# Performance work log

Hardware: AMD Instinct MI355X
Metric: run time of the kernel (lower is better)

## Reference

```python
import jax, jax.numpy as jnp
import numpy as np

N_NODES = 100000
N_EDGES = 3200000
N_GRAPHS = 64


def _gcn_conv(x, W, b, row, col, norm, n):
    # GCNConv: linear transform, then normalized scatter-add aggregation, then bias
    h = x @ W                                  # [N, H]
    msg = h[row] * norm[:, None]               # gather + scale, [E+N, H]
    out = jax.ops.segment_sum(msg, col, num_segments=n)
    return out + b


def setup_inputs() -> dict:
    key = jax.random.key(0)
    ks = jax.random.split(key, 8)
    x = jax.random.normal(ks[0], (N_NODES, 128), dtype=jnp.float32)
    edge_index = jax.random.randint(ks[1], (2, N_EDGES), 0, N_NODES, dtype=jnp.int64)
    batch = jnp.sort(jax.random.randint(ks[2], (N_NODES,), 0, N_GRAPHS, dtype=jnp.int64))
    W1 = jax.random.normal(ks[3], (128, 256), dtype=jnp.float32) * (1.0 / np.sqrt(128))
    b1 = jnp.zeros((256,), dtype=jnp.float32)
    W2 = jax.random.normal(ks[4], (256, 256), dtype=jnp.float32) * (1.0 / np.sqrt(256))
    b2 = jnp.zeros((256,), dtype=jnp.float32)
    Wl = jax.random.normal(ks[5], (256, 2), dtype=jnp.float32) * (1.0 / np.sqrt(256))
    bl = jnp.zeros((2,), dtype=jnp.float32)
    return {"x": x, "edge_index": edge_index, "batch": batch,
            "W1": W1, "b1": b1, "W2": W2, "b2": b2, "Wl": Wl, "bl": bl}


def reference(x, edge_index, batch, W1, b1, W2, b2, Wl, bl):
    n = x.shape[0]
    # add self-loops (PyG GCNConv default)
    loop = jnp.arange(n, dtype=edge_index.dtype)
    row = jnp.concatenate([edge_index[0], loop])   # source
    col = jnp.concatenate([edge_index[1], loop])   # target
    # symmetric normalization: deg computed on targets (with self-loops)
    deg = jax.ops.segment_sum(jnp.ones_like(col, dtype=x.dtype), col, num_segments=n)
    dinv = jnp.where(deg > 0, jax.lax.rsqrt(deg), 0.0)
    norm = dinv[row] * dinv[col]

    h = jax.nn.relu(_gcn_conv(x, W1, b1, row, col, norm, n))
    # dropout p=0.1 is identity at inference (training=False)
    h = jax.nn.relu(_gcn_conv(h, W2, b2, row, col, norm, n))

    # global mean pool over graphs
    sums = jax.ops.segment_sum(h, batch, num_segments=N_GRAPHS)
    cnts = jax.ops.segment_sum(jnp.ones((n,), dtype=h.dtype), batch, num_segments=N_GRAPHS)
    pooled = sums / jnp.maximum(cnts, 1.0)[:, None]

    return pooled @ Wl + bl
```

## Files before the change

### kernel.cpp

```cpp
#include <hip/hip_runtime.h>
#include <hip/hip_bf16.h>
#include <cstddef>

#define NODES  100000
#define EDGES  3200000
#define ETOT   3300000
#define NGRAPH 64
#define HDIM   256
#define BSHIFT 9
#define NBUCK  196
#define BCAP   19456

typedef __hip_bfloat16 bf16;
typedef short bf16x8 __attribute__((ext_vector_type(8)));
typedef float f32x4 __attribute__((ext_vector_type(4)));
typedef float f32x2 __attribute__((ext_vector_type(2)));
typedef unsigned u32x2 __attribute__((ext_vector_type(2)));
typedef unsigned u32x4 __attribute__((ext_vector_type(4)));

__device__ __forceinline__ float blo(unsigned u) { return __uint_as_float(u << 16); }
__device__ __forceinline__ float bhi(unsigned u) { return __uint_as_float(u & 0xffff0000u); }

__global__ void xcast_kernel(const float* __restrict__ x, bf16* __restrict__ xb) {
    int i = blockIdx.x * 256 + threadIdx.x;
    if ((size_t)i * 4 >= (size_t)NODES * 128) return;
    float4 v = *(const float4*)(x + (size_t)i * 4);
    union { __hip_bfloat162 h[2]; uint2 u; } pk;
    pk.h[0] = __float22bfloat162_rn(make_float2(v.x, v.y));
    pk.h[1] = __float22bfloat162_rn(make_float2(v.z, v.w));
    *(uint2*)(xb + (size_t)i * 4) = pk.u;
}

__global__ void wcast_kernel(const float* __restrict__ W1, const float* __restrict__ W2,
                             bf16* __restrict__ W1t, bf16* __restrict__ W2t) {
    int i = blockIdx.x * 256 + threadIdx.x;
    if (i < 128 * 256) {
        int n = i / 128, k = i - n * 128;
        W1t[i] = __float2bfloat16(W1[(size_t)k * 256 + n]);
    } else if (i < 128 * 256 + 256 * 256) {
        int q = i - 128 * 256;
        int n = q / 256, k = q - n * 256;
        W2t[q] = __float2bfloat16(W2[(size_t)k * 256 + n]);
    }
}

__global__ __launch_bounds__(1024) void fillp1_kernel(const int* __restrict__ row,
                                                      const int* __restrict__ col,
                                                      int* __restrict__ gcnt,
                                                      uint2* __restrict__ recs) {
    __shared__ int hist[NBUCK];
    __shared__ int base[NBUCK];
    int t = threadIdx.x;
    if (t < NBUCK) hist[t] = 0;
    __syncthreads();
    int e0 = blockIdx.x * 16384;
    int r[16], c[16], rk[16];
    #pragma unroll
    for (int i = 0; i < 16; i++) {
        int e = e0 + i * 1024 + t;
        r[i] = -1;
        if (e < ETOT) {
            if (e < EDGES) { r[i] = row[e]; c[i] = col[e]; }
            else           { r[i] = e - EDGES; c[i] = r[i]; }
            rk[i] = atomicAdd(&hist[c[i] >> BSHIFT], 1);
        }
    }
    __syncthreads();
    if (t < NBUCK && hist[t] > 0) base[t] = atomicAdd(&gcnt[t], hist[t]);
    __syncthreads();
    #pragma unroll
    for (int i = 0; i < 16; i++) {
        if (r[i] >= 0) {
            int b = c[i] >> BSHIFT;
            recs[(size_t)b * BCAP + base[b] + rk[i]] = make_uint2((unsigned)r[i], (unsigned)c[i]);
        }
    }
}

__global__ void bscan_kernel(const int* __restrict__ gcnt, int* __restrict__ bbase) {
    __shared__ int part[256];
    int t = threadIdx.x;
    int v0 = (t < NBUCK) ? gcnt[t] : 0;
    part[t] = v0;
    __syncthreads();
    for (int off = 1; off < 256; off <<= 1) {
        int v = (t >= off) ? part[t - off] : 0;
        __syncthreads();
        part[t] += v;
        __syncthreads();
    }
    if (t < NBUCK) bbase[t] = part[t] - v0;
}

__global__ __launch_bounds__(256) void build_kernel(const uint2* __restrict__ recs,
                                                    const int* __restrict__ gcnt,
                                                    const int* __restrict__ bbase,
                                                    int* __restrict__ rowptr,
                                                    float* __restrict__ dinv,
                                                    int* __restrict__ csr) {
    __shared__ int hist[512];
    __shared__ int cur[512];
    __shared__ int part[256];
    const int b = blockIdx.x, t = threadIdx.x;
    const int n0 = b << BSHIFT;
    const int cnt = gcnt[b];
    const int base = bbase[b];
    hist[t] = 0; hist[t + 256] = 0;
    __syncthreads();
    const uint2* rb = recs + (size_t)b * BCAP;
    for (int i = t; i < cnt; i += 256) atomicAdd(&hist[(int)rb[i].y - n0], 1);
    __syncthreads();
    int h0 = hist[2 * t], h1 = hist[2 * t + 1];
    part[t] = h0 + h1;
    __syncthreads();
    for (int off = 1; off < 256; off <<= 1) {
        int v = (t >= off) ? part[t - off] : 0;
        __syncthreads();
        part[t] += v;
        __syncthreads();
    }
    int ex = (t == 0) ? 0 : part[t - 1];
    cur[2 * t]     = ex;
    cur[2 * t + 1] = ex + h0;
    int v0 = n0 + 2 * t, v1 = v0 + 1;
    if (v0 < NODES) { rowptr[v0] = base + ex;      dinv[v0] = rsqrtf((float)h0); }
    if (v1 < NODES) { rowptr[v1] = base + ex + h0; dinv[v1] = rsqrtf((float)h1); }
    if (b == 0 && t == 0) rowptr[NODES] = ETOT;
    __syncthreads();
    for (int i = t; i < cnt; i += 256) {
        uint2 r = rb[i];
        int pos = atomicAdd(&cur[(int)r.y - n0], 1);
        csr[base + pos] = (int)r.x;
    }
}

__global__ void agg1_kernel(const bf16* __restrict__ xb, const int* __restrict__ rowptr,
                            const int* __restrict__ csr, const float* __restrict__ dinv,
                            bf16* __restrict__ out) {
    int w    = (blockIdx.x * blockDim.x + threadIdx.x) >> 6;
    int lane = threadIdx.x & 63;
    int half = lane >> 5, li = lane & 31;
    int node = w * 2 + half;
    if (node >= NODES) return;
    int beg = rowptr[node], end = rowptr[node + 1];
    float a0 = 0.f, a1 = 0.f, a2 = 0.f, a3 = 0.f;
    int j = beg;
    for (; j + 1 < end; j += 2) {
        int s0 = csr[j], s1 = csr[j + 1];
        float w0 = dinv[s0], w1 = dinv[s1];
        uint2 q0 = *(const uint2*)(xb + (size_t)s0 * 128 + li * 4);
        uint2 q1 = *(const uint2*)(xb + (size_t)s1 * 128 + li * 4);
        a0 += w0 * blo(q0.x) + w1 * blo(q1.x);
        a1 += w0 * bhi(q0.x) + w1 * bhi(q1.x);
        a2 += w0 * blo(q0.y) + w1 * blo(q1.y);
        a3 += w0 * bhi(q0.y) + w1 * bhi(q1.y);
    }
    if (j < end) {
        int s0 = csr[j];
        float w0 = dinv[s0];
        uint2 q0 = *(const uint2*)(xb + (size_t)s0 * 128 + li * 4);
        a0 += w0 * blo(q0.x);
        a1 += w0 * bhi(q0.x);
        a2 += w0 * blo(q0.y);
        a3 += w0 * bhi(q0.y);
    }
    float d = dinv[node];
    union { __hip_bfloat162 h[2]; uint2 u; } pk;
    pk.h[0] = __float22bfloat162_rn(make_float2(a0 * d, a1 * d));
    pk.h[1] = __float22bfloat162_rn(make_float2(a2 * d, a3 * d));
    *(uint2*)(out + (size_t)node * 128 + li * 4) = pk.u;
}

__global__ void agg2_kernel(const unsigned char* __restrict__ h8, const int* __restrict__ rowptr,
                            const int* __restrict__ csr, const float* __restrict__ dinv,
                            bf16* __restrict__ out) {
    int w    = (blockIdx.x * blockDim.x + threadIdx.x) >> 6;
    int lane = threadIdx.x & 63;
    int half = lane >> 5, li = lane & 31;
    int node = w * 2 + half;
    if (node >= NODES) return;
    int beg = rowptr[node], end = rowptr[node + 1];
    float a[8] = {};
    int j = beg;
#define ACC8(q, wv) do {                                                   \
        f32x2 d0 = __builtin_amdgcn_cvt_pk_f32_fp8((int)(q).x, false);     \
        f32x2 d1 = __builtin_amdgcn_cvt_pk_f32_fp8((int)(q).x, true);      \
        f32x2 d2 = __builtin_amdgcn_cvt_pk_f32_fp8((int)(q).y, false);     \
        f32x2 d3 = __builtin_amdgcn_cvt_pk_f32_fp8((int)(q).y, true);      \
        a[0] += (wv) * d0.x; a[1] += (wv) * d0.y;                          \
        a[2] += (wv) * d1.x; a[3] += (wv) * d1.y;                          \
        a[4] += (wv) * d2.x; a[5] += (wv) * d2.y;                          \
        a[6] += (wv) * d3.x; a[7] += (wv) * d3.y;                          \
    } while (0)
    for (; j + 3 < end; j += 4) {
        int s0 = csr[j], s1 = csr[j + 1], s2 = csr[j + 2], s3 = csr[j + 3];
        float w0 = dinv[s0], w1 = dinv[s1], w2 = dinv[s2], w3 = dinv[s3];
        u32x2 q0 = *(const u32x2*)(h8 + (size_t)s0 * 256 + li * 8);
        u32x2 q1 = *(const u32x2*)(h8 + (size_t)s1 * 256 + li * 8);
        u32x2 q2 = *(const u32x2*)(h8 + (size_t)s2 * 256 + li * 8);
        u32x2 q3 = *(const u32x2*)(h8 + (size_t)s3 * 256 + li * 8);
        ACC8(q0, w0); ACC8(q1, w1); ACC8(q2, w2); ACC8(q3, w3);
    }
    for (; j < end; j++) {
        int s0 = csr[j];
        float w0 = dinv[s0];
        u32x2 q0 = *(const u32x2*)(h8 + (size_t)s0 * 256 + li * 8);
        ACC8(q0, w0);
    }
#undef ACC8
    float d = dinv[node];
    union { __hip_bfloat162 h[4]; u32x4 u; } pk;
    pk.h[0] = __float22bfloat162_rn(make_float2(a[0] * d, a[1] * d));
    pk.h[1] = __float22bfloat162_rn(make_float2(a[2] * d, a[3] * d));
    pk.h[2] = __float22bfloat162_rn(make_float2(a[4] * d, a[5] * d));
    pk.h[3] = __float22bfloat162_rn(make_float2(a[6] * d, a[7] * d));
    *(u32x4*)(out + (size_t)node * 256 + li * 8) = pk.u;
}

template <int K, bool OUT_FP8>
__global__ __launch_bounds__(256) void mgemm_kernel(const bf16* __restrict__ A,
                                                    const bf16* __restrict__ Bt,
                                                    const float* __restrict__ bias,
                                                    bf16* __restrict__ Cb,
                                                    unsigned char* __restrict__ C8) {
    __shared__ short As[128][40];
    __shared__ short Bs[128][40];
    const int t    = threadIdx.x;
    const int bm   = (int)(blockIdx.x >> 1) * 128;
    const int bn   = (int)(blockIdx.x & 1) * 128;
    const int lane = t & 63;
    const int wave = t >> 6;
    const int wm   = (wave >> 1) * 64, wn = (wave & 1) * 64;
    const int m16  = lane & 15, kq = lane >> 4;
    f32x4 acc[4][4] = {};

    for (int k0 = 0; k0 < K; k0 += 32) {
        #pragma unroll
        for (int h = 0; h < 2; h++) {
            int q = t * 2 + h;
            int rr = q >> 2, seg = q & 3;
            uint4 va = {0u, 0u, 0u, 0u};
            int grow = bm + rr;
            if (grow < NODES) va = *(const uint4*)(A + (size_t)grow * K + k0 + seg * 8);
            *(uint4*)&As[rr][seg * 8] = va;
            uint4 vb = *(const uint4*)(Bt + (size_t)(bn + rr) * K + k0 + seg * 8);
            *(uint4*)&Bs[rr][seg * 8] = vb;
        }
        __syncthreads();
        bf16x8 af[4], bf_[4];
        #pragma unroll
        for (int i = 0; i < 4; i++) {
            af[i]  = *(const bf16x8*)&As[wm + i * 16 + m16][kq * 8];
            bf_[i] = *(const bf16x8*)&Bs[wn + i * 16 + m16][kq * 8];
        }
        #pragma unroll
        for (int mt = 0; mt < 4; mt++)
            #pragma unroll
            for (int nt = 0; nt < 4; nt++)
                acc[mt][nt] = __builtin_amdgcn_mfma_f32_16x16x32_bf16(af[mt], bf_[nt],
                                                                     acc[mt][nt], 0, 0, 0);
        __syncthreads();
    }

    #pragma unroll
    for (int mt = 0; mt < 4; mt++) {
        #pragma unroll
        for (int r = 0; r < 4; r++) {
            int row = bm + wm + mt * 16 + kq * 4 + r;
            if (row >= NODES) continue;
            #pragma unroll
            for (int nt = 0; nt < 4; nt++) {
                int colb = bn + wn + nt * 16 + m16;
                float v = fmaxf(acc[mt][nt][r] + bias[colb], 0.f);
                if (OUT_FP8) {
                    int pkd = __builtin_amdgcn_cvt_pk_fp8_f32(v, v, 0, false);
                    C8[(size_t)row * 256 + colb] = (unsigned char)(pkd & 0xff);
                } else {
                    Cb[(size_t)row * 256 + colb] = __float2bfloat16(v);
                }
            }
        }
    }
}

__global__ void pool_kernel(const bf16* __restrict__ h2, const int* __restrict__ batch,
                            float* __restrict__ sums) {
    int lane = threadIdx.x & 63;
    int sub  = threadIdx.x >> 6;
    int col  = blockIdx.y * 64 + lane;
    int r0   = blockIdx.x * 1024 + sub * 256;
    if (r0 >= NODES) return;
    int r1 = r0 + 256; if (r1 > NODES) r1 = NODES;
    float acc = 0.f;
    int g = batch[r0];
    for (int r = r0; r < r1; r++) {
        int gg = batch[r];
        if (gg != g) { atomicAdd(&sums[g * 256 + col], acc); acc = 0.f; g = gg; }
        acc += __bfloat162float(h2[(size_t)r * 256 + col]);
    }
    atomicAdd(&sums[g * 256 + col], acc);
}

__global__ void final_kernel(const float* __restrict__ sums, const int* __restrict__ batch,
                             const float* __restrict__ Wl, const float* __restrict__ bl,
                             float* __restrict__ out) {
    int g = blockIdx.x;
    int l = threadIdx.x;
    int lo = 0, hi = NODES;
    while (lo < hi) { int m = (lo + hi) >> 1; if (batch[m] < g) lo = m + 1; else hi = m; }
    int lb = lo;
    lo = lb; hi = NODES;
    while (lo < hi) { int m = (lo + hi) >> 1; if (batch[m] <= g) lo = m + 1; else hi = m; }
    int cnt = lo - lb;
    float inv = 1.f / fmaxf((float)cnt, 1.f);
    float a0 = 0.f, a1 = 0.f;
    for (int k = l; k < 256; k += 64) {
        float p = sums[g * 256 + k] * inv;
        a0 += p * Wl[k * 2 + 0];
        a1 += p * Wl[k * 2 + 1];
    }
    for (int off = 32; off > 0; off >>= 1) {
        a0 += __shfl_down(a0, off, 64);
        a1 += __shfl_down(a1, off, 64);
    }
    if (l == 0) {
        out[g * 2 + 0] = a0 + bl[0];
        out[g * 2 + 1] = a1 + bl[1];
    }
}

extern "C" void kernel_launch(void* const* d_in, const int* in_sizes, int n_in,
                              void* d_out, int out_size, void* d_ws, size_t ws_size,
                              hipStream_t stream) {
    const float* x    = (const float*)d_in[0];
    const int*   ei   = (const int*)d_in[1];
    const int*   bat  = (const int*)d_in[2];
    const float* W1   = (const float*)d_in[3];
    const float* b1   = (const float*)d_in[4];
    const float* W2   = (const float*)d_in[5];
    const float* b2   = (const float*)d_in[6];
    const float* Wl   = (const float*)d_in[7];
    const float* bl   = (const float*)d_in[8];
    float*       out  = (float*)d_out;
    const int* erow = ei;
    const int* ecol = ei + EDGES;

    char* p = (char*)d_ws;
    auto take = [&](size_t bytes) {
        char* r = p;
        p += (bytes + 255) & ~(size_t)255;
        return r;
    };
    float* dinv   = (float*)take((size_t)NODES * 4);
    int*   rowptr = (int*)  take((size_t)(NODES + 1) * 4);
    int*   gcnt   = (int*)  take((size_t)NBUCK * 4);
    int*   bbase  = (int*)  take((size_t)NBUCK * 4);
    int*   csr    = (int*)  take((size_t)ETOT * 4);
    float* sums   = (float*)take((size_t)NGRAPH * HDIM * 4);
    bf16*  W1t    = (bf16*) take((size_t)128 * 256 * 2);
    bf16*  W2t    = (bf16*) take((size_t)256 * 256 * 2);
    char*  reg1   = (char*) take((size_t)NODES * HDIM * 2);
    char*  reg2   = (char*) take((size_t)NODES * HDIM * 2);
    char*  reg3   = (char*) take((size_t)NODES * HDIM * 2);
    bf16*          xb      = (bf16*)reg1;
    unsigned char* h1f8    = (unsigned char*)reg1;
    bf16*          aggbuf1 = (bf16*)reg2;
    bf16*          aggbuf2 = (bf16*)reg2;
    uint2*         recs    = (uint2*)reg3;
    bf16*          h2b     = (bf16*)reg3;

    hipMemsetAsync(sums, 0, (size_t)NGRAPH * HDIM * 4, stream);
    hipMemsetAsync(gcnt, 0, (size_t)NBUCK * 4, stream);
    xcast_kernel<<<(NODES * 128 / 4 + 255) / 256, 256, 0, stream>>>(x, xb);
    wcast_kernel<<<(128 * 256 + 256 * 256 + 255) / 256, 256, 0, stream>>>(W1, W2, W1t, W2t);

    fillp1_kernel<<<(ETOT + 16383) / 16384, 1024, 0, stream>>>(erow, ecol, gcnt, recs);
    bscan_kernel <<<1, 256, 0, stream>>>(gcnt, bbase);
    build_kernel <<<NBUCK, 256, 0, stream>>>(recs, gcnt, bbase, rowptr, dinv, csr);

    const int AGG_BLOCKS = (NODES / 2 * 64) / 256;
    agg1_kernel<<<AGG_BLOCKS, 256, 0, stream>>>(xb, rowptr, csr, dinv, aggbuf1);

    const int MB = (NODES + 127) / 128;
    mgemm_kernel<128, true ><<<MB * 2, 256, 0, stream>>>(aggbuf1, W1t, b1, nullptr, h1f8);

    agg2_kernel<<<AGG_BLOCKS, 256, 0, stream>>>(h1f8, rowptr, csr, dinv, aggbuf2);

    mgemm_kernel<256, false><<<MB * 2, 256, 0, stream>>>(aggbuf2, W2t, b2, h2b, nullptr);

    pool_kernel<<<dim3((NODES + 1023) / 1024, 4), 256, 0, stream>>>(h2b, bat, sums);

    final_kernel<<<NGRAPH, 64, 0, stream>>>(sums, bat, Wl, bl, out);
}
```

Before: 626.0 us.

## Store input features and layer-2 output in fp8, split fill histogram four ways

Casts the input features to fp8 instead of bf16, so the first aggregation gathers half as many bytes per edge, and unrolls its edge loop by four. The second GEMM now writes fp8 instead of bf16, and pooling reads four fp8 values per lane. The bucket fill kernel spreads its shared-memory histogram atomics over four copies to reduce contention. These cuts in gather and write traffic cost extra quantization error on the input features and the final hidden state.

Result: faster. 560.8 us (-10.4%).

```diff
diff --git a/kernel.cpp b/kernel.cpp
--- a/kernel.cpp
+++ b/kernel.cpp
@@ -18,17 +18,13 @@
 typedef unsigned u32x2 __attribute__((ext_vector_type(2)));
 typedef unsigned u32x4 __attribute__((ext_vector_type(4)));
 
-__device__ __forceinline__ float blo(unsigned u) { return __uint_as_float(u << 16); }
-__device__ __forceinline__ float bhi(unsigned u) { return __uint_as_float(u & 0xffff0000u); }
-
-__global__ void xcast_kernel(const float* __restrict__ x, bf16* __restrict__ xb) {
+__global__ void xcast_kernel(const float* __restrict__ x, unsigned char* __restrict__ x8) {
     int i = blockIdx.x * 256 + threadIdx.x;
     if ((size_t)i * 4 >= (size_t)NODES * 128) return;
     float4 v = *(const float4*)(x + (size_t)i * 4);
-    union { __hip_bfloat162 h[2]; uint2 u; } pk;
-    pk.h[0] = __float22bfloat162_rn(make_float2(v.x, v.y));
-    pk.h[1] = __float22bfloat162_rn(make_float2(v.z, v.w));
-    *(uint2*)(xb + (size_t)i * 4) = pk.u;
+    int w = __builtin_amdgcn_cvt_pk_fp8_f32(v.x, v.y, 0, false);
+    w     = __builtin_amdgcn_cvt_pk_fp8_f32(v.z, v.w, w, true);
+    *(unsigned*)(x8 + (size_t)i * 4) = (unsigned)w;
 }
 
 __global__ void wcast_kernel(const float* __restrict__ W1, const float* __restrict__ W2,
@@ -48,10 +44,12 @@
                                                       const int* __restrict__ col,
                                                       int* __restrict__ gcnt,
                                                       uint2* __restrict__ recs) {
-    __shared__ int hist[NBUCK];
+    __shared__ int hist[4][NBUCK];
+    __shared__ int coff[4][NBUCK];
     __shared__ int base[NBUCK];
-    int t = threadIdx.x;
-    if (t < NBUCK) hist[t] = 0;
+    int t  = threadIdx.x;
+    int cp = t & 3;
+    for (int i = t; i < 4 * NBUCK; i += 1024) ((int*)hist)[i] = 0;
     __syncthreads();
     int e0 = blockIdx.x * 16384;
     int r[16], c[16], rk[16];
@@ -62,17 +60,23 @@
         if (e < ETOT) {
             if (e < EDGES) { r[i] = row[e]; c[i] = col[e]; }
             else           { r[i] = e - EDGES; c[i] = r[i]; }
-            rk[i] = atomicAdd(&hist[c[i] >> BSHIFT], 1);
-        }
-    }
-    __syncthreads();
-    if (t < NBUCK && hist[t] > 0) base[t] = atomicAdd(&gcnt[t], hist[t]);
+            rk[i] = atomicAdd(&hist[cp][c[i] >> BSHIFT], 1);
+        }
+    }
+    __syncthreads();
+    if (t < NBUCK) {
+        int h0 = hist[0][t], h1 = hist[1][t], h2 = hist[2][t], h3 = hist[3][t];
+        coff[0][t] = 0; coff[1][t] = h0; coff[2][t] = h0 + h1; coff[3][t] = h0 + h1 + h2;
+        int tot = h0 + h1 + h2 + h3;
+        base[t] = (tot > 0) ? atomicAdd(&gcnt[t], tot) : 0;
+    }
     __syncthreads();
     #pragma unroll
     for (int i = 0; i < 16; i++) {
         if (r[i] >= 0) {
             int b = c[i] >> BSHIFT;
-            recs[(size_t)b * BCAP + base[b] + rk[i]] = make_uint2((unsigned)r[i], (unsigned)c[i]);
+            recs[(size_t)b * BCAP + base[b] + coff[cp][b] + rk[i]] =
+                make_uint2((unsigned)r[i], (unsigned)c[i]);
         }
     }
 }
@@ -134,7 +138,7 @@
     }
 }
 
-__global__ void agg1_kernel(const bf16* __restrict__ xb, const int* __restrict__ rowptr,
+__global__ void agg1_kernel(const unsigned char* __restrict__ x8, const int* __restrict__ rowptr,
                             const int* __restrict__ csr, const float* __restrict__ dinv,
                             bf16* __restrict__ out) {
     int w    = (blockIdx.x * blockDim.x + threadIdx.x) >> 6;
@@ -145,30 +149,33 @@
     int beg = rowptr[node], end = rowptr[node + 1];
     float a0 = 0.f, a1 = 0.f, a2 = 0.f, a3 = 0.f;
     int j = beg;
-    for (; j + 1 < end; j += 2) {
-        int s0 = csr[j], s1 = csr[j + 1];
-        float w0 = dinv[s0], w1 = dinv[s1];
-        uint2 q0 = *(const uint2*)(xb + (size_t)s0 * 128 + li * 4);
-        uint2 q1 = *(const uint2*)(xb + (size_t)s1 * 128 + li * 4);
-        a0 += w0 * blo(q0.x) + w1 * blo(q1.x);
-        a1 += w0 * bhi(q0.x) + w1 * bhi(q1.x);
-        a2 += w0 * blo(q0.y) + w1 * blo(q1.y);
-        a3 += w0 * bhi(q0.y) + w1 * bhi(q1.y);
-    }
-    if (j < end) {
+#define ACC4(q, wv) do {                                                   \
+        f32x2 d0 = __builtin_amdgcn_cvt_pk_f32_fp8((int)(q), false);       \
+        f32x2 d1 = __builtin_amdgcn_cvt_pk_f32_fp8((int)(q), true);        \
+        a0 += (wv) * d0.x; a1 += (wv) * d0.y;                              \
+        a2 += (wv) * d1.x; a3 += (wv) * d1.y;                              \
+    } while (0)
+    for (; j + 3 < end; j += 4) {
+        int s0 = csr[j], s1 = csr[j + 1], s2 = csr[j + 2], s3 = csr[j + 3];
+        float w0 = dinv[s0], w1 = dinv[s1], w2 = dinv[s2], w3 = dinv[s3];
+        unsigned q0 = *(const unsigned*)(x8 + (size_t)s0 * 128 + li * 4);
+        unsigned q1 = *(const unsigned*)(x8 + (size_t)s1 * 128 + li * 4);
+        unsigned q2 = *(const unsigned*)(x8 + (size_t)s2 * 128 + li * 4);
+        unsigned q3 = *(const unsigned*)(x8 + (size_t)s3 * 128 + li * 4);
+        ACC4(q0, w0); ACC4(q1, w1); ACC4(q2, w2); ACC4(q3, w3);
+    }
+    for (; j < end; j++) {
         int s0 = csr[j];
         float w0 = dinv[s0];
-        uint2 q0 = *(const uint2*)(xb + (size_t)s0 * 128 + li * 4);
-        a0 += w0 * blo(q0.x);
-        a1 += w0 * bhi(q0.x);
-        a2 += w0 * blo(q0.y);
-        a3 += w0 * bhi(q0.y);
-    }
+        unsigned q0 = *(const unsigned*)(x8 + (size_t)s0 * 128 + li * 4);
+        ACC4(q0, w0);
+    }
+#undef ACC4
     float d = dinv[node];
-    union { __hip_bfloat162 h[2]; uint2 u; } pk;
+    union { __hip_bfloat162 h[2]; u32x2 u; } pk;
     pk.h[0] = __float22bfloat162_rn(make_float2(a0 * d, a1 * d));
     pk.h[1] = __float22bfloat162_rn(make_float2(a2 * d, a3 * d));
-    *(uint2*)(out + (size_t)node * 128 + li * 4) = pk.u;
+    *(u32x2*)(out + (size_t)node * 128 + li * 4) = pk.u;
 }
 
 __global__ void agg2_kernel(const unsigned char* __restrict__ h8, const int* __restrict__ rowptr,
@@ -217,11 +224,10 @@
     *(u32x4*)(out + (size_t)node * 256 + li * 8) = pk.u;
 }
 
-template <int K, bool OUT_FP8>
+template <int K>
 __global__ __launch_bounds__(256) void mgemm_kernel(const bf16* __restrict__ A,
                                                     const bf16* __restrict__ Bt,
                                                     const float* __restrict__ bias,
-                                                    bf16* __restrict__ Cb,
                                                     unsigned char* __restrict__ C8) {
     __shared__ short As[128][40];
     __shared__ short Bs[128][40];
@@ -272,33 +278,41 @@
             for (int nt = 0; nt < 4; nt++) {
                 int colb = bn + wn + nt * 16 + m16;
                 float v = fmaxf(acc[mt][nt][r] + bias[colb], 0.f);
-                if (OUT_FP8) {
-                    int pkd = __builtin_amdgcn_cvt_pk_fp8_f32(v, v, 0, false);
-                    C8[(size_t)row * 256 + colb] = (unsigned char)(pkd & 0xff);
-                } else {
-                    Cb[(size_t)row * 256 + colb] = __float2bfloat16(v);
-                }
+                int pkd = __builtin_amdgcn_cvt_pk_fp8_f32(v, v, 0, false);
+                C8[(size_t)row * 256 + colb] = (unsigned char)(pkd & 0xff);
             }
         }
     }
 }
 
-__global__ void pool_kernel(const bf16* __restrict__ h2, const int* __restrict__ batch,
+__global__ void pool_kernel(const unsigned char* __restrict__ h2, const int* __restrict__ batch,
                             float* __restrict__ sums) {
     int lane = threadIdx.x & 63;
     int sub  = threadIdx.x >> 6;
-    int col  = blockIdx.y * 64 + lane;
     int r0   = blockIdx.x * 1024 + sub * 256;
     if (r0 >= NODES) return;
     int r1 = r0 + 256; if (r1 > NODES) r1 = NODES;
-    float acc = 0.f;
+    float a0 = 0.f, a1 = 0.f, a2 = 0.f, a3 = 0.f;
     int g = batch[r0];
+    int cb = lane * 4;
     for (int r = r0; r < r1; r++) {
         int gg = batch[r];
-        if (gg != g) { atomicAdd(&sums[g * 256 + col], acc); acc = 0.f; g = gg; }
-        acc += __bfloat162float(h2[(size_t)r * 256 + col]);
-    }
-    atomicAdd(&sums[g * 256 + col], acc);
+        if (gg != g) {
+            atomicAdd(&sums[g * 256 + cb + 0], a0);
+            atomicAdd(&sums[g * 256 + cb + 1], a1);
+            atomicAdd(&sums[g * 256 + cb + 2], a2);
+            atomicAdd(&sums[g * 256 + cb + 3], a3);
+            a0 = a1 = a2 = a3 = 0.f; g = gg;
+        }
+        unsigned q = *(const unsigned*)(h2 + (size_t)r * 256 + cb);
+        f32x2 d0 = __builtin_amdgcn_cvt_pk_f32_fp8((int)q, false);
+        f32x2 d1 = __builtin_amdgcn_cvt_pk_f32_fp8((int)q, true);
+        a0 += d0.x; a1 += d0.y; a2 += d1.x; a3 += d1.y;
+    }
+    atomicAdd(&sums[g * 256 + cb + 0], a0);
+    atomicAdd(&sums[g * 256 + cb + 1], a1);
+    atomicAdd(&sums[g * 256 + cb + 2], a2);
+    atomicAdd(&sums[g * 256 + cb + 3], a3);
 }
 
 __global__ void final_kernel(const float* __restrict__ sums, const int* __restrict__ batch,
@@ -359,19 +373,19 @@
     float* sums   = (float*)take((size_t)NGRAPH * HDIM * 4);
     bf16*  W1t    = (bf16*) take((size_t)128 * 256 * 2);
     bf16*  W2t    = (bf16*) take((size_t)256 * 256 * 2);
-    char*  reg1   = (char*) take((size_t)NODES * HDIM * 2);
+    char*  reg1   = (char*) take((size_t)NODES * HDIM * 1);
     char*  reg2   = (char*) take((size_t)NODES * HDIM * 2);
-    char*  reg3   = (char*) take((size_t)NODES * HDIM * 2);
-    bf16*          xb      = (bf16*)reg1;
+    char*  reg3   = (char*) take((size_t)NBUCK * BCAP * 8);
+    unsigned char* x8      = (unsigned char*)reg1;
     unsigned char* h1f8    = (unsigned char*)reg1;
     bf16*          aggbuf1 = (bf16*)reg2;
     bf16*          aggbuf2 = (bf16*)reg2;
     uint2*         recs    = (uint2*)reg3;
-    bf16*          h2b     = (bf16*)reg3;
+    unsigned char* h2f8    = (unsigned char*)reg3;
 
     hipMemsetAsync(sums, 0, (size_t)NGRAPH * HDIM * 4, stream);
     hipMemsetAsync(gcnt, 0, (size_t)NBUCK * 4, stream);
-    xcast_kernel<<<(NODES * 128 / 4 + 255) / 256, 256, 0, stream>>>(x, xb);
+    xcast_kernel<<<(NODES * 128 / 4 + 255) / 256, 256, 0, stream>>>(x, x8);
     wcast_kernel<<<(128 * 256 + 256 * 256 + 255) / 256, 256, 0, stream>>>(W1, W2, W1t, W2t);
 
     fillp1_kernel<<<(ETOT + 16383) / 16384, 1024, 0, stream>>>(erow, ecol, gcnt, recs);
@@ -379,16 +393,16 @@
     build_kernel <<<NBUCK, 256, 0, stream>>>(recs, gcnt, bbase, rowptr, dinv, csr);
 
     const int AGG_BLOCKS = (NODES / 2 * 64) / 256;
-    agg1_kernel<<<AGG_BLOCKS, 256, 0, stream>>>(xb, rowptr, csr, dinv, aggbuf1);
+    agg1_kernel<<<AGG_BLOCKS, 256, 0, stream>>>(x8, rowptr, csr, dinv, aggbuf1);
 
     const int MB = (NODES + 127) / 128;
-    mgemm_kernel<128, true ><<<MB * 2, 256, 0, stream>>>(aggbuf1, W1t, b1, nullptr, h1f8);
+    mgemm_kernel<128><<<MB * 2, 256, 0, stream>>>(aggbuf1, W1t, b1, h1f8);
 
     agg2_kernel<<<AGG_BLOCKS, 256, 0, stream>>>(h1f8, rowptr, csr, dinv, aggbuf2);
 
-    mgemm_kernel<256, false><<<MB * 2, 256, 0, stream>>>(aggbuf2, W2t, b2, h2b, nullptr);
-
-    pool_kernel<<<dim3((NODES + 1023) / 1024, 4), 256, 0, stream>>>(h2b, bat, sums);
+    mgemm_kernel<256><<<MB * 2, 256, 0, stream>>>(aggbuf2, W2t, b2, h2f8);
+
+    pool_kernel<<<(NODES + 1023) / 1024, 256, 0, stream>>>(h2f8, bat, sums);
 
     final_kernel<<<NGRAPH, 64, 0, stream>>>(sums, bat, Wl, bl, out);
 }
```
